# Kernel tuning notes

Hardware: AMD Instinct MI355X
Metric: run time of the kernel (lower is better)

The kernel has to match this reference:

```python
import jax, jax.numpy as jnp
import numpy as np

HID = 1024; NH = 4; HD = HID // NH; KS = 4; C = 64; EPS = 1e-05
B = 4; L = 4096


def setup_inputs():
    key = jax.random.key(0)
    ks = jax.random.split(key, 9)
    return {
        "x": jax.random.normal(ks[0], (B, L, HID), jnp.float32),
        "Wq": jax.random.normal(ks[1], (HID, HID), jnp.float32) * 0.02,
        "Wk": jax.random.normal(ks[2], (HID, HID), jnp.float32) * 0.02,
        "Wv": jax.random.normal(ks[3], (HID, HID), jnp.float32) * 0.02,
        "Wb": jax.random.normal(ks[4], (HID, NH), jnp.float32) * 0.02,
        "conv_q": jax.random.normal(ks[5], (HID, 1, KS), jnp.float32) * 0.5,
        "conv_k": jax.random.normal(ks[6], (HID, 1, KS), jnp.float32) * 0.5,
        "conv_v": jax.random.normal(ks[7], (HID, 1, KS), jnp.float32) * 0.5,
        "g": jnp.ones((HD,), jnp.float32),
        "Wo": jax.random.normal(ks[8], (HID, HID), jnp.float32) * 0.02,
    }


def _causal_dwconv(x, w):
    # x: (B, L, Ch); w: (Ch, 1, K). Depthwise causal conv (left pad K-1) + SiLU,
    # equivalent to torch Conv1d(padding=K-1) followed by right-truncation.
    xc = jnp.moveaxis(x, 1, 2)  # (B, Ch, L)
    y = jax.lax.conv_general_dilated(
        xc, w, window_strides=(1,), padding=[(w.shape[-1] - 1, 0)],
        dimension_numbers=("NCH", "OIH", "NCH"), feature_group_count=w.shape[0])
    return jnp.moveaxis(jax.nn.silu(y), 1, 2)


def _forward(x, Wq, Wk, Wv, Wb, conv_q, conv_k, conv_v, g, Wo):
    Bx, Lx, _ = x.shape
    N = Lx // C  # num chunks (L chosen divisible by C)
    q = _causal_dwconv(x @ Wq, conv_q).reshape(Bx, Lx, NH, HD)
    k = _causal_dwconv(x @ Wk, conv_k).reshape(Bx, Lx, NH, HD)
    v = _causal_dwconv(x @ Wv, conv_v).reshape(Bx, Lx, NH, HD)
    # kq_norm: L2-normalize each head vector over head_dim
    q = q / jnp.linalg.norm(q, axis=-1, keepdims=True)
    k = k / jnp.linalg.norm(k, axis=-1, keepdims=True)
    beta = jax.nn.sigmoid(x @ Wb)  # (B, L, H)
    Q = q.reshape(Bx, N, C, NH, HD)
    K = k.reshape(Bx, N, C, NH, HD)
    V = v.reshape(Bx, N, C, NH, HD)
    bta = beta.reshape(Bx, N, C, NH, 1)
    Kb = K * bta
    Vb = V * bta
    # T = eye(C) - sum_h tril(Kb_h @ K_h^T, -1)  (T shared across heads, as in source)
    A = jnp.einsum("bnihd,bnjhd->bnij", Kb, K)
    T0 = jnp.eye(C, dtype=x.dtype) - jnp.tril(A, -1)
    col = jnp.arange(C)

    def body(i, T):
        # Replicates: T[:,:,i,:i] += (T[:,:,i,:,None] * T[:,:,:,:i]).sum(-2)
        row = jax.lax.dynamic_slice_in_dim(T, i, 1, axis=2)[:, :, 0]  # (B,N,C)
        acc = jnp.einsum("bnj,bnjc->bnc", row, T)
        new_row = jnp.where(col < i, row + acc, row)
        return jax.lax.dynamic_update_slice_in_dim(T, new_row[:, :, None, :], i, axis=2)

    T = jax.lax.fori_loop(1, C, body, T0)
    W = jnp.einsum("bnij,bnjhd->bnihd", T, Kb)
    U = jnp.einsum("bnij,bnjhd->bnihd", T, Vb)

    def chunk_step(S, inp):
        q_i, k_i, w_i, u0 = inp  # each (B, C, H, D)
        # source einsum 'bchd,bhdd->bchd' extracts the diagonal of S
        Sd = jnp.diagonal(S, axis1=-2, axis2=-1)  # (B, H, D)
        u_i = u0 - w_i * Sd[:, None]
        o_inter = q_i * Sd[:, None]
        # source: einsum('bchd,bchd->bc', q, k).tril() -- tril over the (B, C) matrix
        A_i = jnp.tril(jnp.einsum("bchd,bchd->bc", q_i, k_i))
        o_intra = A_i[:, :, None, None] * u_i
        S = S + jnp.einsum("bchd,bche->bhde", k_i, u_i)
        return S, o_inter + o_intra

    xs = tuple(jnp.moveaxis(a, 1, 0) for a in (Q, K, W, U))  # (N, B, C, H, D)
    S0 = jnp.zeros((Bx, NH, HD, HD), x.dtype)
    S, O = jax.lax.scan(chunk_step, S0, xs)
    o = jnp.moveaxis(O, 0, 1).reshape(Bx, Lx, NH, HD)
    # RMSNorm over head_dim with learned scale g
    o = o * jax.lax.rsqrt(jnp.mean(o * o, axis=-1, keepdims=True) + EPS) * g
    out = o.reshape(Bx, Lx, NH * HD) @ Wo
    return out, S


def reference(x, Wq, Wk, Wv, Wb, conv_q, conv_k, conv_v, g, Wo):
    return _forward(x, Wq, Wk, Wv, Wb, conv_q, conv_k, conv_v, g, Wo)
```

## Files before the change

kernel.cpp:

```cpp
#include <hip/hip_runtime.h>
#include <hip/hip_bf16.h>

#define HID 1024
#define NH 4
#define HD 256
#define NCH 64
#define BB 4
#define LL 4096
#define ROWS (BB*LL)
#define SSIZE (BB*NH*HD*HD)

typedef __hip_bfloat16 bf16;
typedef __attribute__((ext_vector_type(8))) short short8;
typedef __attribute__((ext_vector_type(4))) float f32x4;

struct u16x4 { unsigned short x, y, z, w; };

__device__ __forceinline__ float bfu2f(unsigned short u) {
  return __uint_as_float(((unsigned int)u) << 16);
}
__device__ __forceinline__ unsigned short f2bfu(float f) {
  unsigned int x = __float_as_uint(f);
  return (unsigned short)((x + 0x7FFFu + ((x >> 16) & 1u)) >> 16);
}
__device__ __forceinline__ float ldv(const float* p) { return *p; }
__device__ __forceinline__ float ldv(const bf16* p) { return bfu2f(*(const unsigned short*)p); }
__device__ __forceinline__ float4 ld4(const float* p) { return *(const float4*)p; }
__device__ __forceinline__ float4 ld4(const bf16* p) {
  u16x4 u = *(const u16x4*)p;
  return make_float4(bfu2f(u.x), bfu2f(u.y), bfu2f(u.z), bfu2f(u.w));
}
__device__ __forceinline__ void st4(float* p, float4 v) { *(float4*)p = v; }
__device__ __forceinline__ void st4(bf16* p, float4 v) {
  u16x4 u; u.x = f2bfu(v.x); u.y = f2bfu(v.y); u.z = f2bfu(v.z); u.w = f2bfu(v.w);
  *(u16x4*)p = u;
}
__device__ __forceinline__ void stc(float* C, size_t i, float v) { C[i] = v; }
__device__ __forceinline__ void stc(bf16* C, size_t i, float v) {
  ((unsigned short*)C)[i] = f2bfu(v);
}

typedef const __attribute__((address_space(1))) unsigned int* gptr_t;
typedef __attribute__((address_space(3))) unsigned int* lptr_t;
__device__ __forceinline__ void gload16(const void* g, void* l) {
  __builtin_amdgcn_global_load_lds((gptr_t)g, (lptr_t)l, 16, 0, 0);
}


template <typename OT>
__device__ __forceinline__
void gemm_body(const unsigned short* __restrict__ A,
               const unsigned short* __restrict__ Bt, OT* __restrict__ C,
               int m0, int n0, unsigned short* Asl, unsigned short* Bsl) {
  const int tid = threadIdx.x;
  const int wave = tid >> 6, lane = tid & 63;
  const int wr = wave >> 1, wc = wave & 1;
  f32x4 acc[4][4] = {};
  const int cA = (wave << 6) + lane;
  for (int k0 = 0; k0 < HID; k0 += 32) {
#pragma unroll
    for (int i = 0; i < 2; ++i) {
      int c = cA + (i << 8);
      int row = c >> 2, ko = (c & 3) << 3;
      gload16(&A[(size_t)(m0 + row) * HID + k0 + ko],
              &Asl[(size_t)((i << 8) + (wave << 6)) * 8]);
      gload16(&Bt[(size_t)(n0 + row) * HID + k0 + ko],
              &Bsl[(size_t)((i << 8) + (wave << 6)) * 8]);
    }
    __syncthreads();
    short8 af[4], bfr[4];
#pragma unroll
    for (int f = 0; f < 4; ++f) {
      int ra = (wr << 6) + (f << 4) + (lane & 15);
      af[f] = *(const short8*)&Asl[ra * 32 + ((lane >> 4) << 3)];
      int rb = (wc << 6) + (f << 4) + (lane & 15);
      bfr[f] = *(const short8*)&Bsl[rb * 32 + ((lane >> 4) << 3)];
    }
#pragma unroll
    for (int i = 0; i < 4; ++i)
#pragma unroll
      for (int j = 0; j < 4; ++j)
        acc[i][j] = __builtin_amdgcn_mfma_f32_16x16x32_bf16(af[i], bfr[j],
                                                            acc[i][j], 0, 0, 0);
    __syncthreads();
  }
#pragma unroll
  for (int i = 0; i < 4; ++i) {
    int r0 = m0 + (wr << 6) + (i << 4) + ((lane >> 4) << 2);
#pragma unroll
    for (int j = 0; j < 4; ++j) {
      int c0 = n0 + (wc << 6) + (j << 4) + (lane & 15);
#pragma unroll
      for (int r = 0; r < 4; ++r)
        stc(C, (size_t)(r0 + r) * HID + c0, acc[i][j][r]);
    }
  }
}

template <int MODE, typename IT, typename ST>
__device__ __forceinline__
void conv8_body(const IT* __restrict__ lin, const float* __restrict__ w,
                const float* __restrict__ beta, ST* __restrict__ out, int row0) {
  const int tid = threadIdx.x;
  const int ch = tid << 2;
  const int h = tid >> 6;
  float wv[4][4];
#pragma unroll
  for (int j = 0; j < 4; ++j) {
    float4 t4 = *(const float4*)&w[(ch + j) << 2];
    wv[j][0] = t4.x; wv[j][1] = t4.y; wv[j][2] = t4.z; wv[j][3] = t4.w;
  }
  const int l0 = row0 & (LL - 1);
  const bool hasprev = (l0 != 0);
  float4 xw0, xw1, xw2, xw3;
  const float4 z4 = make_float4(0.f, 0.f, 0.f, 0.f);
  xw0 = hasprev ? ld4(&lin[(size_t)(row0 - 3) * HID + ch]) : z4;
  xw1 = hasprev ? ld4(&lin[(size_t)(row0 - 2) * HID + ch]) : z4;
  xw2 = hasprev ? ld4(&lin[(size_t)(row0 - 1) * HID + ch]) : z4;
#pragma unroll
  for (int r = 0; r < 8; ++r) {
    const int gr = row0 + r;
    xw3 = ld4(&lin[(size_t)gr * HID + ch]);
    float y[4];
#pragma unroll
    for (int j = 0; j < 4; ++j) {
      float xv0 = j == 0 ? xw0.x : j == 1 ? xw0.y : j == 2 ? xw0.z : xw0.w;
      float xv1 = j == 0 ? xw1.x : j == 1 ? xw1.y : j == 2 ? xw1.z : xw1.w;
      float xv2 = j == 0 ? xw2.x : j == 1 ? xw2.y : j == 2 ? xw2.z : xw2.w;
      float xv3 = j == 0 ? xw3.x : j == 1 ? xw3.y : j == 2 ? xw3.z : xw3.w;
      y[j] = xv0 * wv[j][0] + xv1 * wv[j][1] + xv2 * wv[j][2] + xv3 * wv[j][3];
      y[j] = y[j] / (1.f + expf(-y[j]));
    }
    float scale;
    if (MODE < 2) {
      float ss = y[0]*y[0] + y[1]*y[1] + y[2]*y[2] + y[3]*y[3];
#pragma unroll
      for (int off = 32; off; off >>= 1) ss += __shfl_xor(ss, off);
      scale = 1.f / sqrtf(ss);
    } else {
      scale = beta[(gr << 2) + h];
    }
    st4(&out[(size_t)gr * HID + ch],
        make_float4(y[0]*scale, y[1]*scale, y[2]*scale, y[3]*scale));
    xw0 = xw1; xw1 = xw2; xw2 = xw3;
  }
}


__global__ __launch_bounds__(256)
void prep_convT(const float* __restrict__ x, const float* __restrict__ Wb,
                const float* __restrict__ Wq, const float* __restrict__ Wv,
                const float* __restrict__ Wo, const float* __restrict__ Wk,
                bf16* __restrict__ hi, bf16* __restrict__ lo,
                float* __restrict__ beta,
                unsigned short* __restrict__ Wqt, unsigned short* __restrict__ Wvt,
                unsigned short* __restrict__ Wot, unsigned short* __restrict__ Wkht,
                unsigned short* __restrict__ Wklt) {
  __shared__ float t[64][65];
  const int bx = blockIdx.x;
  const int tid = threadIdx.x;
  if (bx < 4096) {
    const int wave = tid >> 6, lane = tid & 63;
    const int m = (bx << 2) + wave;
    float a0 = 0.f, a1 = 0.f, a2 = 0.f, a3 = 0.f;
#pragma unroll
    for (int it = 0; it < 4; ++it) {
      int f4 = (it << 6) + lane;
      size_t e = (size_t)m * 256 + f4;
      float4 v = *(const float4*)&x[e << 2];
      u16x4 h; h.x = f2bfu(v.x); h.y = f2bfu(v.y); h.z = f2bfu(v.z); h.w = f2bfu(v.w);
      *(u16x4*)&hi[e << 2] = h;
      u16x4 l;
      l.x = f2bfu(v.x - bfu2f(h.x)); l.y = f2bfu(v.y - bfu2f(h.y));
      l.z = f2bfu(v.z - bfu2f(h.z)); l.w = f2bfu(v.w - bfu2f(h.w));
      *(u16x4*)&lo[e << 2] = l;
      const float xs[4] = {v.x, v.y, v.z, v.w};
#pragma unroll
      for (int j = 0; j < 4; ++j) {
        float4 wb = *(const float4*)&Wb[((f4 << 2) + j) << 2];
        a0 += xs[j] * wb.x; a1 += xs[j] * wb.y;
        a2 += xs[j] * wb.z; a3 += xs[j] * wb.w;
      }
    }
#pragma unroll
    for (int off = 32; off; off >>= 1) {
      a0 += __shfl_xor(a0, off); a1 += __shfl_xor(a1, off);
      a2 += __shfl_xor(a2, off); a3 += __shfl_xor(a3, off);
    }
    if (lane == 0) {
      float4 r;
      r.x = 1.f / (1.f + expf(-a0)); r.y = 1.f / (1.f + expf(-a1));
      r.z = 1.f / (1.f + expf(-a2)); r.w = 1.f / (1.f + expf(-a3));
      *(float4*)&beta[m << 2] = r;
    }
  } else {
    const int idx = bx - 4096;
    const int z = idx >> 8;
    const int xy = idx & 255;
    const int kt = (xy & 15) << 6, nt = (xy >> 4) << 6;
    const float* W = z == 0 ? Wq : z == 1 ? Wv : z == 2 ? Wo : Wk;
#pragma unroll
    for (int i = 0; i < 16; ++i) {
      int id2 = tid + (i << 8);
      int r = id2 >> 6, c = id2 & 63;
      t[r][c] = W[(size_t)(kt + r) * HID + nt + c];
    }
    __syncthreads();
    if (z < 3) {
      unsigned short* Wt = z == 0 ? Wqt : z == 1 ? Wvt : Wot;
#pragma unroll
      for (int i = 0; i < 16; ++i) {
        int id2 = tid + (i << 8);
        int n = id2 >> 6, kk = id2 & 63;
        Wt[(size_t)(nt + n) * HID + kt + kk] = f2bfu(t[kk][n]);
      }
    } else {
#pragma unroll
      for (int i = 0; i < 16; ++i) {
        int id2 = tid + (i << 8);
        int n = id2 >> 6, kk = id2 & 63;
        float v = t[kk][n];
        unsigned short h = f2bfu(v);
        Wkht[(size_t)(nt + n) * HID + kt + kk] = h;
        Wklt[(size_t)(nt + n) * HID + kt + kk] = f2bfu(v - bfu2f(h));
      }
    }
  }
}

__global__ __launch_bounds__(256)
void mfma_gemm3(const unsigned short* __restrict__ Ah_,
                const unsigned short* __restrict__ Al_,
                const unsigned short* __restrict__ Bh_,
                const unsigned short* __restrict__ Bl_,
                float* __restrict__ C) {
  __shared__ unsigned short Ah[128 * 32];
  __shared__ unsigned short Al[128 * 32];
  __shared__ unsigned short Bh[128 * 32];
  __shared__ unsigned short Bl[128 * 32];
  const int tid = threadIdx.x;
  const int wave = tid >> 6, lane = tid & 63;
  const int m0 = blockIdx.x << 7, n0 = blockIdx.y << 7;
  const int wr = wave >> 1, wc = wave & 1;
  f32x4 acc[4][4] = {};
  const int cA = (wave << 6) + lane;
  for (int k0 = 0; k0 < HID; k0 += 32) {
#pragma unroll
    for (int i = 0; i < 2; ++i) {
      int c = cA + (i << 8);
      int row = c >> 2, ko = (c & 3) << 3;
      size_t ga = (size_t)(m0 + row) * HID + k0 + ko;
      size_t gb = (size_t)(n0 + row) * HID + k0 + ko;
      size_t ldst = (size_t)((i << 8) + (wave << 6)) * 8;
      gload16(&Ah_[ga], &Ah[ldst]);
      gload16(&Al_[ga], &Al[ldst]);
      gload16(&Bh_[gb], &Bh[ldst]);
      gload16(&Bl_[gb], &Bl[ldst]);
    }
    __syncthreads();
    short8 ah[4], al[4], bh[4], bl[4];
#pragma unroll
    for (int f = 0; f < 4; ++f) {
      int ra = ((wr << 6) + (f << 4) + (lane & 15)) * 32 + ((lane >> 4) << 3);
      ah[f] = *(const short8*)&Ah[ra];
      al[f] = *(const short8*)&Al[ra];
      int rb = ((wc << 6) + (f << 4) + (lane & 15)) * 32 + ((lane >> 4) << 3);
      bh[f] = *(const short8*)&Bh[rb];
      bl[f] = *(const short8*)&Bl[rb];
    }
#pragma unroll
    for (int i = 0; i < 4; ++i)
#pragma unroll
      for (int j = 0; j < 4; ++j) {
        f32x4 a = acc[i][j];
        a = __builtin_amdgcn_mfma_f32_16x16x32_bf16(al[i], bh[j], a, 0, 0, 0);
        a = __builtin_amdgcn_mfma_f32_16x16x32_bf16(ah[i], bl[j], a, 0, 0, 0);
        a = __builtin_amdgcn_mfma_f32_16x16x32_bf16(ah[i], bh[j], a, 0, 0, 0);
        acc[i][j] = a;
      }
    __syncthreads();
  }
#pragma unroll
  for (int i = 0; i < 4; ++i) {
    int r0 = m0 + (wr << 6) + (i << 4) + ((lane >> 4) << 2);
#pragma unroll
    for (int j = 0; j < 4; ++j) {
      int c0 = n0 + (wc << 6) + (j << 4) + (lane & 15);
#pragma unroll
      for (int r = 0; r < 4; ++r)
        C[(size_t)(r0 + r) * HID + c0] = acc[i][j][r];
    }
  }
}

__global__ __launch_bounds__(256)
void conv8_k(const float* __restrict__ lin, const float* __restrict__ w,
             const float* __restrict__ beta, float* __restrict__ out) {
  conv8_body<1, float, float>(lin, w, beta, out, blockIdx.x << 3);
}

__global__ __launch_bounds__(256)
void qv_gemm(const unsigned short* __restrict__ A,
             const unsigned short* __restrict__ Wqt,
             const unsigned short* __restrict__ Wvt,
             bf16* __restrict__ linq, bf16* __restrict__ linv) {
  __shared__ unsigned short Asl[128 * 32];
  __shared__ unsigned short Bsl[128 * 32];
  const unsigned short* Bt = blockIdx.z ? Wvt : Wqt;
  bf16* C = blockIdx.z ? linv : linq;
  gemm_body<bf16>(A, Bt, C, blockIdx.x << 7, blockIdx.y << 7, Asl, Bsl);
}

__global__ __launch_bounds__(256)
void convqv_ktrans(const bf16* __restrict__ linq, const bf16* __restrict__ linv,
                   const float* __restrict__ cq, const float* __restrict__ cv,
                   const float* __restrict__ beta, bf16* __restrict__ qbuf,
                   bf16* __restrict__ vbuf, const float* __restrict__ k,
                   unsigned short* __restrict__ kt) {
  __shared__ float t[64][65];
  const int bx = blockIdx.x;
  if (bx < 2048) {
    conv8_body<0, bf16, bf16>(linq, cq, beta, qbuf, bx << 3);
  } else if (bx < 4096) {
    conv8_body<2, bf16, bf16>(linv, cv, beta, vbuf, (bx - 2048) << 3);
  } else {
    const int idx = bx - 4096;
    const int r0 = (idx & 255) << 6, c0 = (idx >> 8) << 6;
    const int tid = threadIdx.x;
#pragma unroll
    for (int i = 0; i < 16; ++i) {
      int id2 = tid + (i << 8);
      int rr = id2 >> 6, cc = id2 & 63;
      t[rr][cc] = k[(size_t)(r0 + rr) * HID + c0 + cc];
    }
    __syncthreads();
#pragma unroll
    for (int i = 0; i < 16; ++i) {
      int id2 = tid + (i << 8);
      int cc = id2 >> 6, rr = id2 & 63;
      kt[(size_t)(c0 + cc) * ROWS + r0 + rr] = f2bfu(t[rr][cc]);
    }
  }
}

__global__ __launch_bounds__(256)
void chunkT_kernel(const float* __restrict__ k, const float* __restrict__ beta,
                   float* __restrict__ Tg) {
  __shared__ float T[64][68];
  __shared__ float S1[64][68];
  __shared__ float S2[64][68];
  __shared__ float row_s[64];
  const int bn = blockIdx.x;
  const size_t base = (size_t)bn * 64 * HID;
  const int tid = threadIdx.x;
  const int tr = tid >> 4, tc = tid & 15;
  float acc[4][4] = {{0.f}};
  for (int d0 = 0; d0 < HID; d0 += 64) {
    const int h = d0 >> 8;
#pragma unroll
    for (int p = 0; p < 4; ++p) {
      int rr = (tid >> 4) + (p << 4);
      int c4 = (tid & 15) << 2;
      float4 a = *(const float4*)&k[base + (size_t)rr * HID + d0 + c4];
      float bta = beta[(((bn << 6) + rr) << 2) + h];
      S2[c4 + 0][rr] = a.x; S2[c4 + 1][rr] = a.y;
      S2[c4 + 2][rr] = a.z; S2[c4 + 3][rr] = a.w;
      S1[c4 + 0][rr] = a.x * bta; S1[c4 + 1][rr] = a.y * bta;
      S1[c4 + 2][rr] = a.z * bta; S1[c4 + 3][rr] = a.w * bta;
    }
    __syncthreads();
#pragma unroll
    for (int dd = 0; dd < 64; ++dd) {
      float4 a = *(const float4*)&S1[dd][tr << 2];
      float4 b = *(const float4*)&S2[dd][tc << 2];
      acc[0][0] += a.x*b.x; acc[0][1] += a.x*b.y; acc[0][2] += a.x*b.z; acc[0][3] += a.x*b.w;
      acc[1][0] += a.y*b.x; acc[1][1] += a.y*b.y; acc[1][2] += a.y*b.z; acc[1][3] += a.y*b.w;
      acc[2][0] += a.z*b.x; acc[2][1] += a.z*b.y; acc[2][2] += a.z*b.z; acc[2][3] += a.z*b.w;
      acc[3][0] += a.w*b.x; acc[3][1] += a.w*b.y; acc[3][2] += a.w*b.z; acc[3][3] += a.w*b.w;
    }
    __syncthreads();
  }
#pragma unroll
  for (int i = 0; i < 4; ++i)
#pragma unroll
    for (int j = 0; j < 4; ++j) {
      int ri = (tr << 2) + i, cj = (tc << 2) + j;
      T[ri][cj] = (ri == cj) ? 1.f : (ri > cj ? -acc[i][j] : 0.f);
    }
  __syncthreads();
  for (int i = 1; i < 64; ++i) {
    if (tid < 64) row_s[tid] = T[i][tid];
    __syncthreads();
    if (tid < 64) {
      float a = 0.f;
#pragma unroll 8
      for (int j = 0; j < 64; ++j) a += row_s[j] * T[j][tid];
      if (tid < i) T[i][tid] = row_s[tid] + a;
    }
    __syncthreads();
  }
#pragma unroll
  for (int ii = 0; ii < 4; ++ii) {
    int off = (tid << 4) + (ii << 2);
    int c = off >> 6, j = off & 63;
    *(float4*)&Tg[(size_t)bn * 4096 + off] = *(const float4*)&T[c][j];
  }
}

__global__ __launch_bounds__(256)
void prct_kernel(const float* __restrict__ k, const bf16* __restrict__ v,
                 const float* __restrict__ beta, const float* __restrict__ Tg,
                 float* __restrict__ P, float* __restrict__ R) {
  __shared__ float Ts[4096];
  __shared__ float bs[64];
  const int bn = blockIdx.x >> 2, h = blockIdx.x & 3;
  const int tid = threadIdx.x;
#pragma unroll
  for (int ii = 0; ii < 4; ++ii) {
    int off = (tid << 4) + (ii << 2);
    *(float4*)&Ts[off] = *(const float4*)&Tg[(size_t)bn * 4096 + off];
  }
  if (tid < 64) bs[tid] = beta[(((bn << 6) + tid) << 2) + h];
  __syncthreads();
  const int ch = (h << 8) + tid;
  const size_t base = (size_t)bn * 64 * HID;
  float ct[64];
#pragma unroll
  for (int j = 0; j < 64; ++j) ct[j] = 0.f;
  for (int c = 0; c < 64; ++c) {
    float kc = k[base + (size_t)c * HID + ch];
#pragma unroll
    for (int j = 0; j < 64; ++j) ct[j] += Ts[(c << 6) + j] * kc;
  }
  float p = 0.f, r = 0.f;
#pragma unroll
  for (int j = 0; j < 64; ++j) {
    float kj = k[base + (size_t)j * HID + ch];
    float vj = ldv(&v[base + (size_t)j * HID + ch]);
    p += bs[j] * kj * ct[j];
    r += vj * ct[j];
  }
  P[(size_t)bn * HID + ch] = p;
  R[(size_t)bn * HID + ch] = r;
}

__global__ __launch_bounds__(256)
void scan_ai(const float* __restrict__ P, const float* __restrict__ R,
             float* __restrict__ Sdp, const bf16* __restrict__ q,
             const float* __restrict__ k, float* __restrict__ Ai) {
  const int bx = blockIdx.x;
  if (bx < 16) {
    const int b = bx >> 2;
    const int ch = ((bx & 3) << 8) + threadIdx.x;
    float S = 0.f;
    float p = P[(size_t)(b << 6) * HID + ch];
    float r = R[(size_t)(b << 6) * HID + ch];
    for (int n = 0; n < 64; ++n) {
      Sdp[(size_t)((n << 2) + b) * HID + ch] = S;
      float pn = 0.f, rn = 0.f;
      if (n < 63) {
        pn = P[(size_t)((b << 6) + n + 1) * HID + ch];
        rn = R[(size_t)((b << 6) + n + 1) * HID + ch];
      }
      S = S * (1.f - p) + r;
      p = pn; r = rn;
    }
  } else {
    const int bn = bx - 16;
    const int b = bn >> 6;
    const int wave = threadIdx.x >> 6, lane = threadIdx.x & 63;
    const size_t roff = ((size_t)bn * 64 + wave) * HID;
    float s = 0.f;
#pragma unroll
    for (int it = 0; it < 4; ++it) {
      int d = (lane << 2) + (it << 8);
      float4 a = ld4(&q[roff + d]);
      float4 b4 = *(const float4*)&k[roff + d];
      s += a.x*b4.x + a.y*b4.y + a.z*b4.z + a.w*b4.w;
    }
#pragma unroll
    for (int off = 32; off; off >>= 1) s += __shfl_xor(s, off);
    if (lane == 0) Ai[(bn << 2) + wave] = (wave <= b) ? s : 0.f;
  }
}

__global__ __launch_bounds__(256)
void ucompute_kernel(const float* __restrict__ k, const bf16* __restrict__ v,
                     const float* __restrict__ beta, const float* __restrict__ Tg,
                     const float* __restrict__ Sdp, unsigned short* __restrict__ Ut) {
  __shared__ float Ts[4096];
  __shared__ float va[64][132];
  __shared__ float bs[64];
  const int bn = blockIdx.x >> 3;
  const int rr2 = blockIdx.x & 7;
  const int h = rr2 >> 1, eh = rr2 & 1;
  const int b = bn >> 6, nl = bn & 63;
  const int tid = threadIdx.x;
#pragma unroll
  for (int ii = 0; ii < 4; ++ii) {
    int off = (tid << 4) + (ii << 2);
    *(float4*)&Ts[off] = *(const float4*)&Tg[(size_t)bn * 4096 + off];
  }
  if (tid < 64) bs[tid] = beta[(((bn << 6) + tid) << 2) + h];
  __syncthreads();
  const size_t base = (size_t)bn * 64 * HID;
  const int ch0 = (h << 8) + (eh << 7);
#pragma unroll
  for (int p = 0; p < 8; ++p) {
    int idx = tid + (p << 8);
    int row = idx >> 5;
    int col4 = (idx & 31) << 2;
    int chg = ch0 + col4;
    float4 sd4 = *(const float4*)&Sdp[(size_t)((nl << 2) + b) * HID + chg];
    float4 k4 = *(const float4*)&k[base + (size_t)row * HID + chg];
    float4 v4 = ld4(&v[base + (size_t)row * HID + chg]);
    float bt = bs[row];
    va[row][col4 + 0] = v4.x - bt * k4.x * sd4.x;
    va[row][col4 + 1] = v4.y - bt * k4.y * sd4.y;
    va[row][col4 + 2] = v4.z - bt * k4.z * sd4.z;
    va[row][col4 + 3] = v4.w - bt * k4.w * sd4.w;
  }
  __syncthreads();
  const int e = tid & 127;
  const int chalf = tid >> 7;
  float acc[32];
#pragma unroll
  for (int c2 = 0; c2 < 32; ++c2) acc[c2] = 0.f;
  for (int j = 0; j < 64; ++j) {
    float vaj = va[j][e];
#pragma unroll
    for (int c2 = 0; c2 < 32; ++c2)
      acc[c2] += Ts[((chalf << 5) + c2) * 64 + j] * vaj;
  }
  const size_t ub = ((size_t)(((b << 2) + h) * HD) + (eh << 7) + e) * LL
                  + (nl << 6) + (chalf << 5);
#pragma unroll
  for (int c4 = 0; c4 < 8; ++c4) {
    u16x4 u;
    u.x = f2bfu(acc[(c4 << 2) + 0]); u.y = f2bfu(acc[(c4 << 2) + 1]);
    u.z = f2bfu(acc[(c4 << 2) + 2]); u.w = f2bfu(acc[(c4 << 2) + 3]);
    *(u16x4*)&Ut[ub + (c4 << 2)] = u;
  }
}

__global__ __launch_bounds__(256)
void o_kernel(bf16* __restrict__ q, const float* __restrict__ Sdp,
              const unsigned short* __restrict__ Ut, const float* __restrict__ Ai,
              const float* __restrict__ g) {
  const int row = blockIdx.x;
  const int b = row >> 12;
  const int l = row & (LL - 1);
  const int n = l >> 6, c = l & 63;
  const int ch = threadIdx.x << 2;
  const size_t ro = (size_t)row * HID;
  float4 qv = ld4(&q[ro + ch]);
  float4 sd = *(const float4*)&Sdp[(size_t)((n << 2) + b) * HID + ch];
  float ox = qv.x*sd.x, oy = qv.y*sd.y, oz = qv.z*sd.z, ow = qv.w*sd.w;
  if (c <= b) {
    int bn = (b << 6) + n;
    float a = Ai[(bn << 2) + c];
    const int h = ch >> 8, e = ch & 255;
    const size_t ub = ((size_t)(((b << 2) + h) * HD) + e) * LL + (n << 6) + c;
    ox += a * bfu2f(Ut[ub + 0 * LL]);
    oy += a * bfu2f(Ut[ub + 1 * LL]);
    oz += a * bfu2f(Ut[ub + 2 * LL]);
    ow += a * bfu2f(Ut[ub + 3 * LL]);
  }
  float ss = ox*ox + oy*oy + oz*oz + ow*ow;
#pragma unroll
  for (int off = 32; off; off >>= 1) ss += __shfl_xor(ss, off);
  float scale = 1.f / sqrtf(ss * (1.f / HD) + 1e-5f);
  float4 gv = *(const float4*)&g[ch & (HD - 1)];
  st4(&q[ro + ch], make_float4(ox*scale*gv.x, oy*scale*gv.y, oz*scale*gv.z, ow*scale*gv.w));
}

__global__ __launch_bounds__(256)
void mfma_gemmS(const unsigned short* __restrict__ At,
                const unsigned short* __restrict__ Bt,
                float* __restrict__ Spart, int ngroups) {
  __shared__ unsigned short Asl[128 * 32];
  __shared__ unsigned short Bsl[128 * 32];
  const int tid = threadIdx.x;
  const int wave = tid >> 6, lane = tid & 63;
  const int m0 = blockIdx.x << 7, n0 = blockIdx.y << 7;
  const int bh = blockIdx.z / ngroups;
  const int ng = blockIdx.z % ngroups;
  const int b = bh >> 2, h = bh & 3;
  const size_t kbase = (size_t)b * LL + (size_t)ng * (LL / ngroups);
  const int wr = wave >> 1, wc = wave & 1;
  f32x4 acc[4][4] = {};
  const int cA = (wave << 6) + lane;
  for (int k0 = 0; k0 < LL / ngroups; k0 += 32) {
#pragma unroll
    for (int i = 0; i < 2; ++i) {
      int c = cA + (i << 8);
      int row = c >> 2, ko = (c & 3) << 3;
      gload16(&At[((size_t)(h * HD + m0 + row)) * ROWS + kbase + k0 + ko],
              &Asl[(size_t)((i << 8) + (wave << 6)) * 8]);
      gload16(&Bt[((size_t)(bh * HD + n0 + row)) * LL + (size_t)ng * (LL / ngroups) + k0 + ko],
              &Bsl[(size_t)((i << 8) + (wave << 6)) * 8]);
    }
    __syncthreads();
    short8 af[4], bfr[4];
#pragma unroll
    for (int f = 0; f < 4; ++f) {
      int ra = (wr << 6) + (f << 4) + (lane & 15);
      af[f] = *(const short8*)&Asl[ra * 32 + ((lane >> 4) << 3)];
      int rb = (wc << 6) + (f << 4) + (lane & 15);
      bfr[f] = *(const short8*)&Bsl[rb * 32 + ((lane >> 4) << 3)];
    }
#pragma unroll
    for (int i = 0; i < 4; ++i)
#pragma unroll
      for (int j = 0; j < 4; ++j)
        acc[i][j] = __builtin_amdgcn_mfma_f32_16x16x32_bf16(af[i], bfr[j],
                                                            acc[i][j], 0, 0, 0);
    __syncthreads();
  }
  float* Cp = Spart + (size_t)ng * SSIZE + (size_t)bh * HD * HD;
#pragma unroll
  for (int i = 0; i < 4; ++i) {
    int r0 = m0 + (wr << 6) + (i << 4) + ((lane >> 4) << 2);
#pragma unroll
    for (int j = 0; j < 4; ++j) {
      int c0 = n0 + (wc << 6) + (j << 4) + (lane & 15);
#pragma unroll
      for (int r = 0; r < 4; ++r)
        Cp[(size_t)(r0 + r) * HD + c0] = acc[i][j][r];
    }
  }
}

__global__ __launch_bounds__(256)
void out_sreduce(const unsigned short* __restrict__ A,
                 const unsigned short* __restrict__ Bt, float* __restrict__ C,
                 const float* __restrict__ Spart, float* __restrict__ Sout,
                 int ngroups) {
  __shared__ unsigned short Asl[128 * 32];
  __shared__ unsigned short Bsl[128 * 32];
  const int bx = blockIdx.x;
  if (bx < 1024) {
    gemm_body<float>(A, Bt, C, (bx >> 3) << 7, (bx & 7) << 7, Asl, Bsl);
  } else {
    size_t i = ((size_t)(bx - 1024) * 256 + threadIdx.x) << 2;
    float4 s = make_float4(0.f, 0.f, 0.f, 0.f);
    for (int g = 0; g < ngroups; ++g) {
      float4 p = *(const float4*)&Spart[(size_t)g * SSIZE + i];
      s.x += p.x; s.y += p.y; s.z += p.z; s.w += p.w;
    }
    *(float4*)&Sout[i] = s;
  }
}

extern "C" void kernel_launch(void* const* d_in, const int* in_sizes, int n_in,
                              void* d_out, int out_size, void* d_ws, size_t ws_size,
                              hipStream_t stream) {
  const float* x  = (const float*)d_in[0];
  const float* Wq = (const float*)d_in[1];
  const float* Wk = (const float*)d_in[2];
  const float* Wv = (const float*)d_in[3];
  const float* Wb = (const float*)d_in[4];
  const float* cq = (const float*)d_in[5];
  const float* ck = (const float*)d_in[6];
  const float* cv = (const float*)d_in[7];
  const float* g  = (const float*)d_in[8];
  const float* Wo = (const float*)d_in[9];
  float* out  = (float*)d_out;
  float* Sout = out + (size_t)ROWS * HID;

  const size_t F = (size_t)ROWS * HID;
  char* w = (char*)d_ws;
  float* kbuf  = (float*)w;  w += F * 4;
  bf16*  xb    = (bf16*)w;   w += F * 2;
  bf16*  qbuf  = (bf16*)w;   w += F * 2;
  bf16*  vbuf  = (bf16*)w;   w += F * 2;
  unsigned short* Wqt  = (unsigned short*)w; w += (size_t)HID * HID * 2;
  unsigned short* Wvt  = (unsigned short*)w; w += (size_t)HID * HID * 2;
  unsigned short* Wot  = (unsigned short*)w; w += (size_t)HID * HID * 2;
  unsigned short* Wkht = (unsigned short*)w; w += (size_t)HID * HID * 2;
  unsigned short* Wklt = (unsigned short*)w; w += (size_t)HID * HID * 2;
  float* Tg    = (float*)w;  w += (size_t)BB * NCH * 4096 * 4;
  float* betab = (float*)w;  w += (size_t)ROWS * NH * 4;
  float* Aib   = (float*)w;  w += (size_t)BB * NCH * 4 * 4;
  float* Pb    = (float*)w;  w += (size_t)BB * NCH * HID * 4;
  float* Rb    = (float*)w;  w += (size_t)BB * NCH * HID * 4;
  float* Sdp   = (float*)w;  w += (size_t)BB * NCH * HID * 4;
  const size_t need = (size_t)(w - (char*)d_ws);
  if (ws_size < need) return;

  dim3 gg(ROWS / 128, HID / 128);
  float* linf = out;
  bf16*  linq = (bf16*)out;
  bf16*  linv = linq + F;
  bf16*  xlo  = qbuf;

  prep_convT<<<4096 + 1024, 256, 0, stream>>>(x, Wb, Wq, Wv, Wo, Wk, xb, xlo,
                                              betab, Wqt, Wvt, Wot, Wkht, Wklt);
  mfma_gemm3<<<gg, 256, 0, stream>>>((const unsigned short*)xb,
                                     (const unsigned short*)xlo, Wkht, Wklt, linf);
  conv8_k<<<ROWS / 8, 256, 0, stream>>>(linf, ck, betab, kbuf);
  qv_gemm<<<dim3(ROWS / 128, HID / 128, 2), 256, 0, stream>>>(
      (const unsigned short*)xb, Wqt, Wvt, linq, linv);
  unsigned short* kt = (unsigned short*)xb;
  convqv_ktrans<<<2048 + 2048 + 4096, 256, 0, stream>>>(linq, linv, cq, cv,
                                                        betab, qbuf, vbuf,
                                                        kbuf, kt);
  chunkT_kernel<<<BB * NCH, 256, 0, stream>>>(kbuf, betab, Tg);
  prct_kernel<<<BB * NCH * NH, 256, 0, stream>>>(kbuf, vbuf, betab, Tg, Pb, Rb);
  scan_ai<<<16 + BB * NCH, 256, 0, stream>>>(Pb, Rb, Sdp, qbuf, kbuf, Aib);
  unsigned short* Ut = (unsigned short*)out;
  ucompute_kernel<<<BB * NCH * NH * 2, 256, 0, stream>>>(kbuf, vbuf, betab, Tg,
                                                         Sdp, Ut);
  o_kernel<<<ROWS, 256, 0, stream>>>(qbuf, Sdp, Ut, Aib, g);
  float* Spart = kbuf;
  const int ngroups = 8;
  mfma_gemmS<<<dim3(2, 2, 16 * ngroups), 256, 0, stream>>>(kt, Ut, Spart, ngroups);
  out_sreduce<<<1024 + SSIZE / 1024, 256, 0, stream>>>(
      (const unsigned short*)qbuf, Wot, out, Spart, Sout, ngroups);
}
```

Baseline: 678.7 us.

## Merge independent kernels into shared launches to overlap small stages

Three pairs of independent kernels are merged into single launches that branch on block index: the Q/V projection GEMM with the chunk T-matrix computation, the P/R computation with the Ai dot products (the scan is split out as its own kernel), and the output normalization with the state GEMM. The aim is to cut launch overhead and let the small, low-occupancy work such as the 256-block chunkT triangular solve and the 512-block state GEMM run alongside larger kernels. In exchange, the shared launches take on the larger shared-memory footprint and register pressure of the heavier branch, and o_gemmS now reads Ut while writing q, which relies on the two branches touching disjoint buffers.

Result: slower. 752.8 us (+10.9%).

```diff
diff --git a/kernel.cpp b/kernel.cpp
--- a/kernel.cpp
+++ b/kernel.cpp
@@ -143,6 +143,69 @@
     st4(&out[(size_t)gr * HID + ch],
         make_float4(y[0]*scale, y[1]*scale, y[2]*scale, y[3]*scale));
     xw0 = xw1; xw1 = xw2; xw2 = xw3;
+  }
+}
+
+__device__ __forceinline__
+void chunkT_body(const float* __restrict__ k, const float* __restrict__ beta,
+                 float* __restrict__ Tg, int bn, float* smem) {
+  float* T  = smem;
+  float* S1 = T + 64 * 68;
+  float* S2 = S1 + 64 * 68;
+  float* row_s = S2 + 64 * 68;
+  const size_t base = (size_t)bn * 64 * HID;
+  const int tid = threadIdx.x;
+  const int tr = tid >> 4, tc = tid & 15;
+  float acc[4][4] = {{0.f}};
+  for (int d0 = 0; d0 < HID; d0 += 64) {
+    const int h = d0 >> 8;
+#pragma unroll
+    for (int p = 0; p < 4; ++p) {
+      int rr = (tid >> 4) + (p << 4);
+      int c4 = (tid & 15) << 2;
+      float4 a = *(const float4*)&k[base + (size_t)rr * HID + d0 + c4];
+      float bta = beta[(((bn << 6) + rr) << 2) + h];
+      S2[(c4 + 0) * 68 + rr] = a.x; S2[(c4 + 1) * 68 + rr] = a.y;
+      S2[(c4 + 2) * 68 + rr] = a.z; S2[(c4 + 3) * 68 + rr] = a.w;
+      S1[(c4 + 0) * 68 + rr] = a.x * bta; S1[(c4 + 1) * 68 + rr] = a.y * bta;
+      S1[(c4 + 2) * 68 + rr] = a.z * bta; S1[(c4 + 3) * 68 + rr] = a.w * bta;
+    }
+    __syncthreads();
+#pragma unroll
+    for (int dd = 0; dd < 64; ++dd) {
+      float4 a = *(const float4*)&S1[dd * 68 + (tr << 2)];
+      float4 b = *(const float4*)&S2[dd * 68 + (tc << 2)];
+      acc[0][0] += a.x*b.x; acc[0][1] += a.x*b.y; acc[0][2] += a.x*b.z; acc[0][3] += a.x*b.w;
+      acc[1][0] += a.y*b.x; acc[1][1] += a.y*b.y; acc[1][2] += a.y*b.z; acc[1][3] += a.y*b.w;
+      acc[2][0] += a.z*b.x; acc[2][1] += a.z*b.y; acc[2][2] += a.z*b.z; acc[2][3] += a.z*b.w;
+      acc[3][0] += a.w*b.x; acc[3][1] += a.w*b.y; acc[3][2] += a.w*b.z; acc[3][3] += a.w*b.w;
+    }
+    __syncthreads();
+  }
+#pragma unroll
+  for (int i = 0; i < 4; ++i)
+#pragma unroll
+    for (int j = 0; j < 4; ++j) {
+      int ri = (tr << 2) + i, cj = (tc << 2) + j;
+      T[ri * 68 + cj] = (ri == cj) ? 1.f : (ri > cj ? -acc[i][j] : 0.f);
+    }
+  __syncthreads();
+  for (int i = 1; i < 64; ++i) {
+    if (tid < 64) row_s[tid] = T[i * 68 + tid];
+    __syncthreads();
+    if (tid < 64) {
+      float a = 0.f;
+#pragma unroll 8
+      for (int j = 0; j < 64; ++j) a += row_s[j] * T[j * 68 + tid];
+      if (tid < i) T[i * 68 + tid] = row_s[tid] + a;
+    }
+    __syncthreads();
+  }
+#pragma unroll
+  for (int ii = 0; ii < 4; ++ii) {
+    int off = (tid << 4) + (ii << 2);
+    int c = off >> 6, j = off & 63;
+    *(float4*)&Tg[(size_t)bn * 4096 + off] = *(const float4*)&T[c * 68 + j];
   }
 }
 
@@ -300,15 +363,25 @@
 }
 
 __global__ __launch_bounds__(256)
-void qv_gemm(const unsigned short* __restrict__ A,
-             const unsigned short* __restrict__ Wqt,
-             const unsigned short* __restrict__ Wvt,
-             bf16* __restrict__ linq, bf16* __restrict__ linv) {
-  __shared__ unsigned short Asl[128 * 32];
-  __shared__ unsigned short Bsl[128 * 32];
-  const unsigned short* Bt = blockIdx.z ? Wvt : Wqt;
-  bf16* C = blockIdx.z ? linv : linq;
-  gemm_body<bf16>(A, Bt, C, blockIdx.x << 7, blockIdx.y << 7, Asl, Bsl);
+void qv_chunkT(const unsigned short* __restrict__ A,
+               const unsigned short* __restrict__ Wqt,
+               const unsigned short* __restrict__ Wvt,
+               bf16* __restrict__ linq, bf16* __restrict__ linv,
+               const float* __restrict__ k, const float* __restrict__ beta,
+               float* __restrict__ Tg) {
+  __shared__ __align__(16) float smem[3 * 64 * 68 + 64];
+  const int bx = blockIdx.x;
+  if (bx < 2048) {
+    const int z = bx >> 10;
+    const int t = bx & 1023;
+    const unsigned short* Bt = z ? Wvt : Wqt;
+    bf16* C = z ? linv : linq;
+    unsigned short* Asl = (unsigned short*)smem;
+    unsigned short* Bsl = Asl + 128 * 32;
+    gemm_body<bf16>(A, Bt, C, (t >> 3) << 7, (t & 7) << 7, Asl, Bsl);
+  } else {
+    chunkT_body(k, beta, Tg, bx - 2048, smem);
+  }
 }
 
 __global__ __launch_bounds__(256)
@@ -344,131 +417,47 @@
 }
 
 __global__ __launch_bounds__(256)
-void chunkT_kernel(const float* __restrict__ k, const float* __restrict__ beta,
-                   float* __restrict__ Tg) {
-  __shared__ float T[64][68];
-  __shared__ float S1[64][68];
-  __shared__ float S2[64][68];
-  __shared__ float row_s[64];
-  const int bn = blockIdx.x;
-  const size_t base = (size_t)bn * 64 * HID;
-  const int tid = threadIdx.x;
-  const int tr = tid >> 4, tc = tid & 15;
-  float acc[4][4] = {{0.f}};
-  for (int d0 = 0; d0 < HID; d0 += 64) {
-    const int h = d0 >> 8;
-#pragma unroll
-    for (int p = 0; p < 4; ++p) {
-      int rr = (tid >> 4) + (p << 4);
-      int c4 = (tid & 15) << 2;
-      float4 a = *(const float4*)&k[base + (size_t)rr * HID + d0 + c4];
-      float bta = beta[(((bn << 6) + rr) << 2) + h];
-      S2[c4 + 0][rr] = a.x; S2[c4 + 1][rr] = a.y;
-      S2[c4 + 2][rr] = a.z; S2[c4 + 3][rr] = a.w;
-      S1[c4 + 0][rr] = a.x * bta; S1[c4 + 1][rr] = a.y * bta;
-      S1[c4 + 2][rr] = a.z * bta; S1[c4 + 3][rr] = a.w * bta;
-    }
-    __syncthreads();
-#pragma unroll
-    for (int dd = 0; dd < 64; ++dd) {
-      float4 a = *(const float4*)&S1[dd][tr << 2];
-      float4 b = *(const float4*)&S2[dd][tc << 2];
-      acc[0][0] += a.x*b.x; acc[0][1] += a.x*b.y; acc[0][2] += a.x*b.z; acc[0][3] += a.x*b.w;
-      acc[1][0] += a.y*b.x; acc[1][1] += a.y*b.y; acc[1][2] += a.y*b.z; acc[1][3] += a.y*b.w;
-      acc[2][0] += a.z*b.x; acc[2][1] += a.z*b.y; acc[2][2] += a.z*b.z; acc[2][3] += a.z*b.w;
-      acc[3][0] += a.w*b.x; acc[3][1] += a.w*b.y; acc[3][2] += a.w*b.z; acc[3][3] += a.w*b.w;
-    }
-    __syncthreads();
-  }
-#pragma unroll
-  for (int i = 0; i < 4; ++i)
-#pragma unroll
-    for (int j = 0; j < 4; ++j) {
-      int ri = (tr << 2) + i, cj = (tc << 2) + j;
-      T[ri][cj] = (ri == cj) ? 1.f : (ri > cj ? -acc[i][j] : 0.f);
-    }
-  __syncthreads();
-  for (int i = 1; i < 64; ++i) {
-    if (tid < 64) row_s[tid] = T[i][tid];
-    __syncthreads();
-    if (tid < 64) {
-      float a = 0.f;
-#pragma unroll 8
-      for (int j = 0; j < 64; ++j) a += row_s[j] * T[j][tid];
-      if (tid < i) T[i][tid] = row_s[tid] + a;
-    }
-    __syncthreads();
-  }
-#pragma unroll
-  for (int ii = 0; ii < 4; ++ii) {
-    int off = (tid << 4) + (ii << 2);
-    int c = off >> 6, j = off & 63;
-    *(float4*)&Tg[(size_t)bn * 4096 + off] = *(const float4*)&T[c][j];
-  }
-}
-
-__global__ __launch_bounds__(256)
-void prct_kernel(const float* __restrict__ k, const bf16* __restrict__ v,
-                 const float* __restrict__ beta, const float* __restrict__ Tg,
-                 float* __restrict__ P, float* __restrict__ R) {
+void prct_ai(const float* __restrict__ k, const bf16* __restrict__ v,
+             const float* __restrict__ beta, const float* __restrict__ Tg,
+             float* __restrict__ P, float* __restrict__ R,
+             const bf16* __restrict__ q, float* __restrict__ Ai) {
   __shared__ float Ts[4096];
   __shared__ float bs[64];
-  const int bn = blockIdx.x >> 2, h = blockIdx.x & 3;
+  const int bx = blockIdx.x;
   const int tid = threadIdx.x;
-#pragma unroll
-  for (int ii = 0; ii < 4; ++ii) {
-    int off = (tid << 4) + (ii << 2);
-    *(float4*)&Ts[off] = *(const float4*)&Tg[(size_t)bn * 4096 + off];
-  }
-  if (tid < 64) bs[tid] = beta[(((bn << 6) + tid) << 2) + h];
-  __syncthreads();
-  const int ch = (h << 8) + tid;
-  const size_t base = (size_t)bn * 64 * HID;
-  float ct[64];
-#pragma unroll
-  for (int j = 0; j < 64; ++j) ct[j] = 0.f;
-  for (int c = 0; c < 64; ++c) {
-    float kc = k[base + (size_t)c * HID + ch];
-#pragma unroll
-    for (int j = 0; j < 64; ++j) ct[j] += Ts[(c << 6) + j] * kc;
-  }
-  float p = 0.f, r = 0.f;
-#pragma unroll
-  for (int j = 0; j < 64; ++j) {
-    float kj = k[base + (size_t)j * HID + ch];
-    float vj = ldv(&v[base + (size_t)j * HID + ch]);
-    p += bs[j] * kj * ct[j];
-    r += vj * ct[j];
-  }
-  P[(size_t)bn * HID + ch] = p;
-  R[(size_t)bn * HID + ch] = r;
-}
-
-__global__ __launch_bounds__(256)
-void scan_ai(const float* __restrict__ P, const float* __restrict__ R,
-             float* __restrict__ Sdp, const bf16* __restrict__ q,
-             const float* __restrict__ k, float* __restrict__ Ai) {
-  const int bx = blockIdx.x;
-  if (bx < 16) {
-    const int b = bx >> 2;
-    const int ch = ((bx & 3) << 8) + threadIdx.x;
-    float S = 0.f;
-    float p = P[(size_t)(b << 6) * HID + ch];
-    float r = R[(size_t)(b << 6) * HID + ch];
-    for (int n = 0; n < 64; ++n) {
-      Sdp[(size_t)((n << 2) + b) * HID + ch] = S;
-      float pn = 0.f, rn = 0.f;
-      if (n < 63) {
-        pn = P[(size_t)((b << 6) + n + 1) * HID + ch];
-        rn = R[(size_t)((b << 6) + n + 1) * HID + ch];
-      }
-      S = S * (1.f - p) + r;
-      p = pn; r = rn;
-    }
+  if (bx < 1024) {
+    const int bn = bx >> 2, h = bx & 3;
+#pragma unroll
+    for (int ii = 0; ii < 4; ++ii) {
+      int off = (tid << 4) + (ii << 2);
+      *(float4*)&Ts[off] = *(const float4*)&Tg[(size_t)bn * 4096 + off];
+    }
+    if (tid < 64) bs[tid] = beta[(((bn << 6) + tid) << 2) + h];
+    __syncthreads();
+    const int ch = (h << 8) + tid;
+    const size_t base = (size_t)bn * 64 * HID;
+    float ct[64];
+#pragma unroll
+    for (int j = 0; j < 64; ++j) ct[j] = 0.f;
+    for (int c = 0; c < 64; ++c) {
+      float kc = k[base + (size_t)c * HID + ch];
+#pragma unroll
+      for (int j = 0; j < 64; ++j) ct[j] += Ts[(c << 6) + j] * kc;
+    }
+    float p = 0.f, r = 0.f;
+#pragma unroll
+    for (int j = 0; j < 64; ++j) {
+      float kj = k[base + (size_t)j * HID + ch];
+      float vj = ldv(&v[base + (size_t)j * HID + ch]);
+      p += bs[j] * kj * ct[j];
+      r += vj * ct[j];
+    }
+    P[(size_t)bn * HID + ch] = p;
+    R[(size_t)bn * HID + ch] = r;
   } else {
-    const int bn = bx - 16;
+    const int bn = bx - 1024;
     const int b = bn >> 6;
-    const int wave = threadIdx.x >> 6, lane = threadIdx.x & 63;
+    const int wave = tid >> 6, lane = tid & 63;
     const size_t roff = ((size_t)bn * 64 + wave) * HID;
     float s = 0.f;
 #pragma unroll
@@ -481,6 +470,26 @@
 #pragma unroll
     for (int off = 32; off; off >>= 1) s += __shfl_xor(s, off);
     if (lane == 0) Ai[(bn << 2) + wave] = (wave <= b) ? s : 0.f;
+  }
+}
+
+__global__ __launch_bounds__(256)
+void scan_kernel(const float* __restrict__ P, const float* __restrict__ R,
+                 float* __restrict__ Sdp) {
+  const int b = blockIdx.x >> 2;
+  const int ch = ((blockIdx.x & 3) << 8) + threadIdx.x;
+  float S = 0.f;
+  float p = P[(size_t)(b << 6) * HID + ch];
+  float r = R[(size_t)(b << 6) * HID + ch];
+  for (int n = 0; n < 64; ++n) {
+    Sdp[(size_t)((n << 2) + b) * HID + ch] = S;
+    float pn = 0.f, rn = 0.f;
+    if (n < 63) {
+      pn = P[(size_t)((b << 6) + n + 1) * HID + ch];
+      rn = R[(size_t)((b << 6) + n + 1) * HID + ch];
+    }
+    S = S * (1.f - p) + r;
+    p = pn; r = rn;
   }
 }
 
@@ -544,89 +553,90 @@
 }
 
 __global__ __launch_bounds__(256)
-void o_kernel(bf16* __restrict__ q, const float* __restrict__ Sdp,
-              const unsigned short* __restrict__ Ut, const float* __restrict__ Ai,
-              const float* __restrict__ g) {
-  const int row = blockIdx.x;
-  const int b = row >> 12;
-  const int l = row & (LL - 1);
-  const int n = l >> 6, c = l & 63;
-  const int ch = threadIdx.x << 2;
-  const size_t ro = (size_t)row * HID;
-  float4 qv = ld4(&q[ro + ch]);
-  float4 sd = *(const float4*)&Sdp[(size_t)((n << 2) + b) * HID + ch];
-  float ox = qv.x*sd.x, oy = qv.y*sd.y, oz = qv.z*sd.z, ow = qv.w*sd.w;
-  if (c <= b) {
-    int bn = (b << 6) + n;
-    float a = Ai[(bn << 2) + c];
-    const int h = ch >> 8, e = ch & 255;
-    const size_t ub = ((size_t)(((b << 2) + h) * HD) + e) * LL + (n << 6) + c;
-    ox += a * bfu2f(Ut[ub + 0 * LL]);
-    oy += a * bfu2f(Ut[ub + 1 * LL]);
-    oz += a * bfu2f(Ut[ub + 2 * LL]);
-    ow += a * bfu2f(Ut[ub + 3 * LL]);
-  }
-  float ss = ox*ox + oy*oy + oz*oz + ow*ow;
-#pragma unroll
-  for (int off = 32; off; off >>= 1) ss += __shfl_xor(ss, off);
-  float scale = 1.f / sqrtf(ss * (1.f / HD) + 1e-5f);
-  float4 gv = *(const float4*)&g[ch & (HD - 1)];
-  st4(&q[ro + ch], make_float4(ox*scale*gv.x, oy*scale*gv.y, oz*scale*gv.z, ow*scale*gv.w));
-}
-
-__global__ __launch_bounds__(256)
-void mfma_gemmS(const unsigned short* __restrict__ At,
-                const unsigned short* __restrict__ Bt,
-                float* __restrict__ Spart, int ngroups) {
+void o_gemmS(bf16* __restrict__ q, const float* __restrict__ Sdp,
+             const unsigned short* __restrict__ Ut, const float* __restrict__ Ai,
+             const float* __restrict__ g, const unsigned short* __restrict__ At,
+             float* __restrict__ Spart, int ngroups) {
   __shared__ unsigned short Asl[128 * 32];
   __shared__ unsigned short Bsl[128 * 32];
+  const int bx = blockIdx.x;
   const int tid = threadIdx.x;
-  const int wave = tid >> 6, lane = tid & 63;
-  const int m0 = blockIdx.x << 7, n0 = blockIdx.y << 7;
-  const int bh = blockIdx.z / ngroups;
-  const int ng = blockIdx.z % ngroups;
-  const int b = bh >> 2, h = bh & 3;
-  const size_t kbase = (size_t)b * LL + (size_t)ng * (LL / ngroups);
-  const int wr = wave >> 1, wc = wave & 1;
-  f32x4 acc[4][4] = {};
-  const int cA = (wave << 6) + lane;
-  for (int k0 = 0; k0 < LL / ngroups; k0 += 32) {
-#pragma unroll
-    for (int i = 0; i < 2; ++i) {
-      int c = cA + (i << 8);
-      int row = c >> 2, ko = (c & 3) << 3;
-      gload16(&At[((size_t)(h * HD + m0 + row)) * ROWS + kbase + k0 + ko],
-              &Asl[(size_t)((i << 8) + (wave << 6)) * 8]);
-      gload16(&Bt[((size_t)(bh * HD + n0 + row)) * LL + (size_t)ng * (LL / ngroups) + k0 + ko],
-              &Bsl[(size_t)((i << 8) + (wave << 6)) * 8]);
-    }
-    __syncthreads();
-    short8 af[4], bfr[4];
-#pragma unroll
-    for (int f = 0; f < 4; ++f) {
-      int ra = (wr << 6) + (f << 4) + (lane & 15);
-      af[f] = *(const short8*)&Asl[ra * 32 + ((lane >> 4) << 3)];
-      int rb = (wc << 6) + (f << 4) + (lane & 15);
-      bfr[f] = *(const short8*)&Bsl[rb * 32 + ((lane >> 4) << 3)];
-    }
-#pragma unroll
-    for (int i = 0; i < 4; ++i)
-#pragma unroll
-      for (int j = 0; j < 4; ++j)
-        acc[i][j] = __builtin_amdgcn_mfma_f32_16x16x32_bf16(af[i], bfr[j],
-                                                            acc[i][j], 0, 0, 0);
-    __syncthreads();
-  }
-  float* Cp = Spart + (size_t)ng * SSIZE + (size_t)bh * HD * HD;
-#pragma unroll
-  for (int i = 0; i < 4; ++i) {
-    int r0 = m0 + (wr << 6) + (i << 4) + ((lane >> 4) << 2);
-#pragma unroll
-    for (int j = 0; j < 4; ++j) {
-      int c0 = n0 + (wc << 6) + (j << 4) + (lane & 15);
-#pragma unroll
-      for (int r = 0; r < 4; ++r)
-        Cp[(size_t)(r0 + r) * HD + c0] = acc[i][j][r];
+  if (bx < 16384) {
+    const int row = bx;
+    const int b = row >> 12;
+    const int l = row & (LL - 1);
+    const int n = l >> 6, c = l & 63;
+    const int ch = tid << 2;
+    const size_t ro = (size_t)row * HID;
+    float4 qv = ld4(&q[ro + ch]);
+    float4 sd = *(const float4*)&Sdp[(size_t)((n << 2) + b) * HID + ch];
+    float ox = qv.x*sd.x, oy = qv.y*sd.y, oz = qv.z*sd.z, ow = qv.w*sd.w;
+    if (c <= b) {
+      int bn = (b << 6) + n;
+      float a = Ai[(bn << 2) + c];
+      const int h = ch >> 8, e = ch & 255;
+      const size_t ub = ((size_t)(((b << 2) + h) * HD) + e) * LL + (n << 6) + c;
+      ox += a * bfu2f(Ut[ub + 0 * LL]);
+      oy += a * bfu2f(Ut[ub + 1 * LL]);
+      oz += a * bfu2f(Ut[ub + 2 * LL]);
+      ow += a * bfu2f(Ut[ub + 3 * LL]);
+    }
+    float ss = ox*ox + oy*oy + oz*oz + ow*ow;
+#pragma unroll
+    for (int off = 32; off; off >>= 1) ss += __shfl_xor(ss, off);
+    float scale = 1.f / sqrtf(ss * (1.f / HD) + 1e-5f);
+    float4 gv = *(const float4*)&g[ch & (HD - 1)];
+    st4(&q[ro + ch], make_float4(ox*scale*gv.x, oy*scale*gv.y, oz*scale*gv.z, ow*scale*gv.w));
+  } else {
+    const int zz = bx - 16384;
+    const int m0 = (zz & 1) << 7, n0 = ((zz >> 1) & 1) << 7;
+    const int zidx = zz >> 2;
+    const int bh = zidx / ngroups;
+    const int ng = zidx % ngroups;
+    const int b = bh >> 2, h = bh & 3;
+    const size_t kbase = (size_t)b * LL + (size_t)ng * (LL / ngroups);
+    const int wave = tid >> 6, lane = tid & 63;
+    const int wr = wave >> 1, wc = wave & 1;
+    f32x4 acc[4][4] = {};
+    const int cA = (wave << 6) + lane;
+    for (int k0 = 0; k0 < LL / ngroups; k0 += 32) {
+#pragma unroll
+      for (int i = 0; i < 2; ++i) {
+        int c = cA + (i << 8);
+        int row = c >> 2, ko = (c & 3) << 3;
+        gload16(&At[((size_t)(h * HD + m0 + row)) * ROWS + kbase + k0 + ko],
+                &Asl[(size_t)((i << 8) + (wave << 6)) * 8]);
+        gload16(&Ut[((size_t)(bh * HD + n0 + row)) * LL + (size_t)ng * (LL / ngroups) + k0 + ko],
+                &Bsl[(size_t)((i << 8) + (wave << 6)) * 8]);
+      }
+      __syncthreads();
+      short8 af[4], bfr[4];
+#pragma unroll
+      for (int f = 0; f < 4; ++f) {
+        int ra = (wr << 6) + (f << 4) + (lane & 15);
+        af[f] = *(const short8*)&Asl[ra * 32 + ((lane >> 4) << 3)];
+        int rb = (wc << 6) + (f << 4) + (lane & 15);
+        bfr[f] = *(const short8*)&Bsl[rb * 32 + ((lane >> 4) << 3)];
+      }
+#pragma unroll
+      for (int i = 0; i < 4; ++i)
+#pragma unroll
+        for (int j = 0; j < 4; ++j)
+          acc[i][j] = __builtin_amdgcn_mfma_f32_16x16x32_bf16(af[i], bfr[j],
+                                                              acc[i][j], 0, 0, 0);
+      __syncthreads();
+    }
+    float* Cp = Spart + (size_t)ng * SSIZE + (size_t)bh * HD * HD;
+#pragma unroll
+    for (int i = 0; i < 4; ++i) {
+      int r0 = m0 + (wr << 6) + (i << 4) + ((lane >> 4) << 2);
+#pragma unroll
+      for (int j = 0; j < 4; ++j) {
+        int c0 = n0 + (wc << 6) + (j << 4) + (lane & 15);
+#pragma unroll
+        for (int r = 0; r < 4; ++r)
+          Cp[(size_t)(r0 + r) * HD + c0] = acc[i][j][r];
+      }
     }
   }
 }
@@ -699,22 +709,22 @@
   mfma_gemm3<<<gg, 256, 0, stream>>>((const unsigned short*)xb,
                                      (const unsigned short*)xlo, Wkht, Wklt, linf);
   conv8_k<<<ROWS / 8, 256, 0, stream>>>(linf, ck, betab, kbuf);
-  qv_gemm<<<dim3(ROWS / 128, HID / 128, 2), 256, 0, stream>>>(
-      (const unsigned short*)xb, Wqt, Wvt, linq, linv);
+  qv_chunkT<<<2048 + BB * NCH, 256, 0, stream>>>((const unsigned short*)xb, Wqt,
+                                                 Wvt, linq, linv, kbuf, betab, Tg);
   unsigned short* kt = (unsigned short*)xb;
   convqv_ktrans<<<2048 + 2048 + 4096, 256, 0, stream>>>(linq, linv, cq, cv,
                                                         betab, qbuf, vbuf,
                                                         kbuf, kt);
-  chunkT_kernel<<<BB * NCH, 256, 0, stream>>>(kbuf, betab, Tg);
-  prct_kernel<<<BB * NCH * NH, 256, 0, stream>>>(kbuf, vbuf, betab, Tg, Pb, Rb);
-  scan_ai<<<16 + BB * NCH, 256, 0, stream>>>(Pb, Rb, Sdp, qbuf, kbuf, Aib);
+  prct_ai<<<1024 + BB * NCH, 256, 0, stream>>>(kbuf, vbuf, betab, Tg, Pb, Rb,
+                                               qbuf, Aib);
+  scan_kernel<<<16, 256, 0, stream>>>(Pb, Rb, Sdp);
   unsigned short* Ut = (unsigned short*)out;
   ucompute_kernel<<<BB * NCH * NH * 2, 256, 0, stream>>>(kbuf, vbuf, betab, Tg,
                                                          Sdp, Ut);
-  o_kernel<<<ROWS, 256, 0, stream>>>(qbuf, Sdp, Ut, Aib, g);
   float* Spart = kbuf;
   const int ngroups = 8;
-  mfma_gemmS<<<dim3(2, 2, 16 * ngroups), 256, 0, stream>>>(kt, Ut, Spart, ngroups);
+  o_gemmS<<<16384 + 512, 256, 0, stream>>>(qbuf, Sdp, Ut, Aib, g, kt, Spart,
+                                           ngroups);
   out_sreduce<<<1024 + SSIZE / 1024, 256, 0, stream>>>(
       (const unsigned short*)qbuf, Wot, out, Spart, Sout, ngroups);
 }
```
